# Kernel optimization log

Hardware: AMD Instinct MI355X
Metric: run time of the kernel (lower is better)

## Reference

```python
import jax, jax.numpy as jnp
import numpy as np

N_NODES = 50000
N_EDGES = 1000000
IN_DIM, HID_DIM, OUT_DIM = 128, 64, 16


def setup_inputs() -> dict:
    key = jax.random.key(0)
    k1, k2, k3, k4 = jax.random.split(key, 4)
    x = jax.random.normal(k1, (N_NODES, IN_DIM), dtype=jnp.float32)
    edge_index = jax.random.randint(k2, (2, N_EDGES), 0, N_NODES, dtype=jnp.int64)
    # Glorot-style scaling for weights, zero bias (PyG GCNConv default init style)
    W1 = jax.random.normal(k3, (IN_DIM, HID_DIM), dtype=jnp.float32) * (1.0 / np.sqrt(IN_DIM))
    b1 = jnp.zeros((HID_DIM,), dtype=jnp.float32)
    W2 = jax.random.normal(k4, (HID_DIM, OUT_DIM), dtype=jnp.float32) * (1.0 / np.sqrt(HID_DIM))
    b2 = jnp.zeros((OUT_DIM,), dtype=jnp.float32)
    return {"x": x, "edge_index": edge_index, "W1": W1, "b1": b1, "W2": W2, "b2": b2}


def gcn_conv(x, src, dst, W, b, num_nodes):
    """PyG GCNConv: add self loops, symmetric deg^{-1/2} normalization,
    linear transform, gather-scale-scatter aggregation, bias."""
    # degree includes self loops (src/dst already augmented by caller)
    deg = jax.ops.segment_sum(jnp.ones_like(dst, dtype=x.dtype), dst, num_segments=num_nodes)
    dinv = jnp.where(deg > 0, deg ** -0.5, 0.0)
    norm = dinv[src] * dinv[dst]            # [E']
    h = x @ W                                # [N, F_out] transform before aggregation
    msg = h[src] * norm[:, None]             # gather + scale
    out = jax.ops.segment_sum(msg, dst, num_segments=num_nodes)  # scatter-add
    return out + b


def reference(x, edge_index, W1, b1, W2, b2):
    n = x.shape[0]
    loops = jnp.arange(n, dtype=edge_index.dtype)
    src = jnp.concatenate([edge_index[0], loops])
    dst = jnp.concatenate([edge_index[1], loops])
    h = gcn_conv(x, src, dst, W1, b1, n)
    h = jax.nn.relu(h)
    out = gcn_conv(h, src, dst, W2, b2, n)
    return out
```

## Files before the change

kernel.cpp:

```cpp
#include <hip/hip_runtime.h>

#define IN_DIM 128
#define HID_DIM 64
#define OUT_DIM 16

#define SSHIFT 7
#define SMASK 127
#define CHUNK 4096
#define CBLK 256
#define KPT (CHUNK / CBLK)
#define CAP 4096

#define G1N 64
#define G1S 132

static __device__ __forceinline__ unsigned short f2bf(float f) {
    unsigned u = __float_as_uint(f);
    unsigned r = u + 0x7fffu + ((u >> 16) & 1u);
    return (unsigned short)(r >> 16);
}
static __device__ __forceinline__ unsigned packbf2(float a, float b) {
    return (unsigned)f2bf(a) | ((unsigned)f2bf(b) << 16);
}
static __device__ __forceinline__ float bflo(unsigned v) { return __uint_as_float(v << 16); }
static __device__ __forceinline__ float bfhi(unsigned v) { return __uint_as_float(v & 0xffff0000u); }

__global__ __launch_bounds__(CBLK) void passC2(const int* __restrict__ src,
                                               const int* __restrict__ dst,
                                               int* __restrict__ gcnt,
                                               int* __restrict__ eb,
                                               int E, int NS) {
    __shared__ int cnt[512];
    __shared__ int bofs[512];
    int t = threadIdx.x;
    for (int s = t; s < NS; s += CBLK) cnt[s] = 0;
    __syncthreads();
    int base = blockIdx.x * CHUNK;
    int dreg[KPT];
    #pragma unroll
    for (int k = 0; k < KPT; ++k) {
        int i = base + k * CBLK + t;
        int d = -1;
        if (i < E) { d = dst[i]; atomicAdd(&cnt[d >> SSHIFT], 1); }
        dreg[k] = d;
    }
    __syncthreads();
    for (int s = t; s < NS; s += CBLK) {
        int c = cnt[s];
        bofs[s] = c ? atomicAdd(&gcnt[s], c) : 0;
        cnt[s] = 0;
    }
    __syncthreads();
    #pragma unroll
    for (int k = 0; k < KPT; ++k) {
        int i = base + k * CBLK + t;
        if (i < E) {
            int d = dreg[k];
            int s = d >> SSHIFT;
            int off = atomicAdd(&cnt[s], 1);
            eb[(size_t)s * CAP + bofs[s] + off] = src[i] | ((d & SMASK) << 17);
        }
    }
}

__global__ __launch_bounds__(256) void passD(const int* __restrict__ eb,
                                             const int* __restrict__ tot,
                                             int* __restrict__ csr_src,
                                             int* __restrict__ row_ptr,
                                             float* __restrict__ dinv,
                                             int N, int E, int NS) {
    __shared__ int red[256];
    __shared__ int deg[128], incl[128], cur[128];
    int s = blockIdx.x, t = threadIdx.x;
    if (t < 128) deg[t] = 0;
    int part = 0;
    for (int k = t; k < s; k += 256) part += tot[k];
    red[t] = part;
    __syncthreads();
    for (int off = 128; off >= 1; off >>= 1) {
        if (t < off) red[t] += red[t + off];
        __syncthreads();
    }
    int b0 = red[0];
    int cnt = tot[s];
    const size_t sbase = (size_t)s * CAP;
    for (int k = t; k < cnt; k += 256) atomicAdd(&deg[eb[sbase + k] >> 17], 1);
    __syncthreads();
    if (t < 128) incl[t] = deg[t];
    __syncthreads();
    for (int off = 1; off < 128; off <<= 1) {
        int tmp = 0;
        if (t < 128 && t >= off) tmp = incl[t - off];
        __syncthreads();
        if (t < 128) incl[t] += tmp;
        __syncthreads();
    }
    if (t < 128) {
        int loff = incl[t] - deg[t];
        cur[t] = b0 + loff;
        int n = (s << SSHIFT) + t;
        if (n < N) {
            row_ptr[n] = b0 + loff;
            dinv[n] = rsqrtf((float)(deg[t] + 1));
        }
    }
    if (s == NS - 1 && t == 0) row_ptr[N] = E;
    __syncthreads();
    for (int k = t; k < cnt; k += 256) {
        int v = eb[sbase + k];
        int dl = v >> 17;
        int p = atomicAdd(&cur[dl], 1);
        csr_src[p] = v & 0x1FFFF;
    }
}

__global__ __launch_bounds__(256) void gemm1_kernel(const float* __restrict__ x,
                                                    const float* __restrict__ W1,
                                                    const float* __restrict__ dinv,
                                                    unsigned* __restrict__ h1u, int N) {
    __shared__ __align__(16) float sW[IN_DIM * HID_DIM];
    __shared__ __align__(16) float sx[G1N * G1S];
    int t = threadIdx.x;
    int node0 = blockIdx.x * G1N;

    const float4* W4  = (const float4*)W1;
    float4*       sW4 = (float4*)sW;
    #pragma unroll
    for (int i = 0; i < 8; ++i) sW4[i * 256 + t] = W4[i * 256 + t];

    const float4* x4 = (const float4*)x;
    for (int i = t; i < G1N * 32; i += 256) {
        int r = i >> 5, c = i & 31;
        int n = node0 + r; if (n >= N) n = 0;
        *(float4*)(sx + r * G1S + c * 4) = x4[(size_t)n * 32 + c];
    }
    __syncthreads();

    int og = t & 15, ng = t >> 4;
    float a00=0.f,a01=0.f,a02=0.f,a03=0.f, a10=0.f,a11=0.f,a12=0.f,a13=0.f,
          a20=0.f,a21=0.f,a22=0.f,a23=0.f, a30=0.f,a31=0.f,a32=0.f,a33=0.f;
    const float* xr = sx + (ng << 2) * G1S;
    #pragma unroll 4
    for (int k = 0; k < IN_DIM; ++k) {
        float x0 = xr[k];
        float x1 = xr[G1S + k];
        float x2 = xr[2 * G1S + k];
        float x3 = xr[3 * G1S + k];
        float4 wv = ((const float4*)(sW + k * HID_DIM))[og];
        a00 = fmaf(x0, wv.x, a00); a01 = fmaf(x0, wv.y, a01);
        a02 = fmaf(x0, wv.z, a02); a03 = fmaf(x0, wv.w, a03);
        a10 = fmaf(x1, wv.x, a10); a11 = fmaf(x1, wv.y, a11);
        a12 = fmaf(x1, wv.z, a12); a13 = fmaf(x1, wv.w, a13);
        a20 = fmaf(x2, wv.x, a20); a21 = fmaf(x2, wv.y, a21);
        a22 = fmaf(x2, wv.z, a22); a23 = fmaf(x2, wv.w, a23);
        a30 = fmaf(x3, wv.x, a30); a31 = fmaf(x3, wv.y, a31);
        a32 = fmaf(x3, wv.z, a32); a33 = fmaf(x3, wv.w, a33);
    }

    int nb = node0 + (ng << 2);
#define G1_STORE(i, c0, c1, c2, c3)                                         \
    {                                                                       \
        int n = nb + i;                                                     \
        if (n <= N) {                                                       \
            float dn = (n < N) ? dinv[n] : 0.f;         \
            uint2 pv;                                                       \
            pv.x = packbf2(c0 * dn, c1 * dn);                               \
            pv.y = packbf2(c2 * dn, c3 * dn);                               \
            ((uint2*)(h1u + (size_t)n * 32))[og] = pv;                      \
        }                                                                   \
    }
    G1_STORE(0, a00, a01, a02, a03)
    G1_STORE(1, a10, a11, a12, a13)
    G1_STORE(2, a20, a21, a22, a23)
    G1_STORE(3, a30, a31, a32, a33)
#undef G1_STORE
}

__global__ __launch_bounds__(256) void agg1_kernel(const unsigned* __restrict__ h1u,
                                                   const int* __restrict__ row_ptr,
                                                   const int* __restrict__ csr_src,
                                                   const float* __restrict__ dinv,
                                                   const float* __restrict__ b1,
                                                   const float* __restrict__ W2,
                                                   unsigned* __restrict__ h2u, int N) {
    __shared__ __align__(16) float sW[OUT_DIM * 68];
    int t = threadIdx.x;
    for (int i = t; i < HID_DIM * OUT_DIM; i += 256) {
        int k = i >> 4, j = i & 15;
        sW[j * 68 + k] = W2[i];
    }
    __syncthreads();

    int lane = t & 63;
    int h  = lane >> 5;
    int l  = lane & 31;
    int es = l >> 3;
    int dg = l & 7;
    int n = blockIdx.x * 8 + ((t >> 6) << 1) + h;
    if (n > N) return;
    if (n == N) {
        if (l < 4) { uint2 z; z.x = 0u; z.y = 0u; ((uint2*)h2u)[(size_t)N * 4 + l] = z; }
        return;
    }

    int e0 = row_ptr[n], e1 = row_ptr[n + 1];
    const uint4* rb = (const uint4*)h1u;
    int sb = h << 5;

    float a0 = 0.f, a1 = 0.f, a2 = 0.f, a3 = 0.f,
          a4 = 0.f, a5 = 0.f, a6 = 0.f, a7 = 0.f;

    for (int base = e0 - 1; base < e1; base += 32) {
        int idx = base + l;
        int sld = N;
        if (idx == e0 - 1) sld = n;
        else if (idx < e1) sld = csr_src[idx];
        int lim = e1 - base;
        if (lim > 32) lim = 32;
        int nr = (lim + 3) >> 2;
        nr = (nr + 1) & ~1;
        for (int r = 0; r < nr; r += 2) {
            int sA = __shfl(sld, sb + ((r + 0) << 2) + es);
            int sB = __shfl(sld, sb + ((r + 1) << 2) + es);
            uint4 vA = rb[(size_t)sA * 8 + dg];
            uint4 vB = rb[(size_t)sB * 8 + dg];
            a0 += bflo(vA.x) + bflo(vB.x);
            a1 += bfhi(vA.x) + bfhi(vB.x);
            a2 += bflo(vA.y) + bflo(vB.y);
            a3 += bfhi(vA.y) + bfhi(vB.y);
            a4 += bflo(vA.z) + bflo(vB.z);
            a5 += bfhi(vA.z) + bfhi(vB.z);
            a6 += bflo(vA.w) + bflo(vB.w);
            a7 += bfhi(vA.w) + bfhi(vB.w);
        }
    }
    #pragma unroll
    for (int m = 8; m <= 16; m <<= 1) {
        a0 += __shfl_xor(a0, m); a1 += __shfl_xor(a1, m);
        a2 += __shfl_xor(a2, m); a3 += __shfl_xor(a3, m);
        a4 += __shfl_xor(a4, m); a5 += __shfl_xor(a5, m);
        a6 += __shfl_xor(a6, m); a7 += __shfl_xor(a7, m);
    }

    float dn = dinv[n];
    float4 bA = ((const float4*)b1)[2 * dg];
    float4 bB = ((const float4*)b1)[2 * dg + 1];
    float r0 = fmaxf(fmaf(dn, a0, bA.x), 0.f);
    float r1 = fmaxf(fmaf(dn, a1, bA.y), 0.f);
    float r2 = fmaxf(fmaf(dn, a2, bA.z), 0.f);
    float r3 = fmaxf(fmaf(dn, a3, bA.w), 0.f);
    float r4 = fmaxf(fmaf(dn, a4, bB.x), 0.f);
    float r5 = fmaxf(fmaf(dn, a5, bB.y), 0.f);
    float r6 = fmaxf(fmaf(dn, a6, bB.z), 0.f);
    float r7 = fmaxf(fmaf(dn, a7, bB.w), 0.f);

    const float* wb = sW + ((es << 2) * 68) + (dg << 3);
    float4 wA, wB2;
    wA = *(const float4*)(wb);        wB2 = *(const float4*)(wb + 4);
    float p0 = r0*wA.x + r1*wA.y + r2*wA.z + r3*wA.w + r4*wB2.x + r5*wB2.y + r6*wB2.z + r7*wB2.w;
    wA = *(const float4*)(wb + 68);   wB2 = *(const float4*)(wb + 72);
    float p1 = r0*wA.x + r1*wA.y + r2*wA.z + r3*wA.w + r4*wB2.x + r5*wB2.y + r6*wB2.z + r7*wB2.w;
    wA = *(const float4*)(wb + 136);  wB2 = *(const float4*)(wb + 140);
    float p2 = r0*wA.x + r1*wA.y + r2*wA.z + r3*wA.w + r4*wB2.x + r5*wB2.y + r6*wB2.z + r7*wB2.w;
    wA = *(const float4*)(wb + 204);  wB2 = *(const float4*)(wb + 208);
    float p3 = r0*wA.x + r1*wA.y + r2*wA.z + r3*wA.w + r4*wB2.x + r5*wB2.y + r6*wB2.z + r7*wB2.w;

    #pragma unroll
    for (int m = 1; m <= 4; m <<= 1) {
        p0 += __shfl_xor(p0, m); p1 += __shfl_xor(p1, m);
        p2 += __shfl_xor(p2, m); p3 += __shfl_xor(p3, m);
    }
    if (dg == 0) {
        uint2 pv;
        pv.x = packbf2(p0 * dn, p1 * dn);
        pv.y = packbf2(p2 * dn, p3 * dn);
        ((uint2*)h2u)[(size_t)n * 4 + es] = pv;
    }
}

__global__ __launch_bounds__(256) void agg2_kernel(const unsigned* __restrict__ h2u,
                                                   const int* __restrict__ row_ptr,
                                                   const int* __restrict__ csr_src,
                                                   const float* __restrict__ dinv,
                                                   const float* __restrict__ b2,
                                                   float* __restrict__ out, int N) {
    int t = threadIdx.x;
    int lane = t & 63;
    int h  = lane >> 4;
    int l  = lane & 15;
    int es = l >> 2;
    int dg = l & 3;
    int n = blockIdx.x * 16 + ((t >> 6) << 2) + h;
    if (n >= N) return;

    int e0 = row_ptr[n], e1 = row_ptr[n + 1];
    const uint2* rb = (const uint2*)h2u;
    int sb = h << 4;

    float a0 = 0.f, a1 = 0.f, a2 = 0.f, a3 = 0.f;

    for (int base = e0 - 1; base < e1; base += 16) {
        int idx = base + l;
        int sld = N;
        if (idx == e0 - 1) sld = n;
        else if (idx < e1) sld = csr_src[idx];
        int lim = e1 - base;
        if (lim > 16) lim = 16;
        int nr = (lim + 3) >> 2;
        nr = (nr + 1) & ~1;
        for (int r = 0; r < nr; r += 2) {
            int sA = __shfl(sld, sb + ((r + 0) << 2) + es);
            int sB = __shfl(sld, sb + ((r + 1) << 2) + es);
            uint2 vA = rb[(size_t)sA * 4 + dg];
            uint2 vB = rb[(size_t)sB * 4 + dg];
            a0 += bflo(vA.x) + bflo(vB.x);
            a1 += bfhi(vA.x) + bfhi(vB.x);
            a2 += bflo(vA.y) + bflo(vB.y);
            a3 += bfhi(vA.y) + bfhi(vB.y);
        }
    }
    #pragma unroll
    for (int m = 4; m <= 8; m <<= 1) {
        a0 += __shfl_xor(a0, m); a1 += __shfl_xor(a1, m);
        a2 += __shfl_xor(a2, m); a3 += __shfl_xor(a3, m);
    }
    if (es == 0) {
        float dn = dinv[n];
        float4 bb = ((const float4*)b2)[dg];
        float4 r;
        r.x = fmaf(dn, a0, bb.x);
        r.y = fmaf(dn, a1, bb.y);
        r.z = fmaf(dn, a2, bb.z);
        r.w = fmaf(dn, a3, bb.w);
        ((float4*)out)[(size_t)n * 4 + dg] = r;
    }
}

extern "C" void kernel_launch(void* const* d_in, const int* in_sizes, int n_in,
                              void* d_out, int out_size, void* d_ws, size_t ws_size,
                              hipStream_t stream) {
    const float* x  = (const float*)d_in[0];
    const int*   ei = (const int*)d_in[1];
    const float* W1 = (const float*)d_in[2];
    const float* b1 = (const float*)d_in[3];
    const float* W2 = (const float*)d_in[4];
    const float* b2 = (const float*)d_in[5];
    float* out = (float*)d_out;

    const int N = in_sizes[0] / IN_DIM;
    const int E = in_sizes[1] / 2;
    const int* src = ei;
    const int* dst = ei + E;

    const int NS  = (N + SMASK) >> SSHIFT;
    const int NSP = NS + 1;
    const int BC  = (E + CHUNK - 1) / CHUNK;

    char* w = (char*)d_ws;
    auto alloc = [&](size_t bytes) -> void* {
        void* p = (void*)w;
        w += (bytes + 255) & ~(size_t)255;
        return p;
    };
    int*      gcnt    = (int*)     alloc((size_t)NSP * 4);
    int*      eb      = (int*)     alloc((size_t)NS * CAP * 4);
    int*      csr_src = (int*)     alloc((size_t)E * 4);
    int*      row_ptr = (int*)     alloc((size_t)(N + 1) * 4);
    float*    dinv    = (float*)   alloc((size_t)N * 4);
    unsigned* h1u     = (unsigned*)alloc((size_t)(N + 1) * 32 * 4);
    unsigned* h2u     = (unsigned*)alloc((size_t)(N + 1) * 8 * 4);

    const int GB  = (N + G1N) / G1N;
    const int AB1 = (N + 8) / 8;
    const int AB2 = (N + 15) / 16;

    hipMemsetAsync(gcnt, 0, (size_t)NSP * 4, stream);
    passC2<<<BC, CBLK, 0, stream>>>(src, dst, gcnt, eb, E, NS);
    passD <<<NS, 256,  0, stream>>>(eb, gcnt, csr_src, row_ptr, dinv, N, E, NS);

    gemm1_kernel<<<GB, 256, 0, stream>>>(x, W1, dinv, h1u, N);
    agg1_kernel<<<AB1, 256, 0, stream>>>(h1u, row_ptr, csr_src, dinv, b1, W2, h2u, N);
    agg2_kernel<<<AB2, 256, 0, stream>>>(h2u, row_ptr, csr_src, dinv, b2, out, N);
}
```

Before: 163.2 us.

## Fuse CSR finalisation with first GEMM via global degree atomics and block specialisation

Per-node degrees are now counted with global atomics inside the bucketing pass, so the first-layer GEMM no longer has to wait for the CSR build to produce dinv. The CSR-finalise kernel and the GEMM are merged into one launch, with blocks split by index between the two roles so they run concurrently. The GEMM tile shrinks to 32 nodes per block to spread more blocks. This removes a launch and a serialisation point, but adds a million global atomics to the bucketing pass and gives the fused kernel a large shared-memory footprint that may lower occupancy for the CSR blocks.

```diff
diff --git a/kernel.cpp b/kernel.cpp
--- a/kernel.cpp
+++ b/kernel.cpp
@@ -11,7 +11,7 @@
 #define KPT (CHUNK / CBLK)
 #define CAP 4096
 
-#define G1N 64
+#define G1N 32
 #define G1S 132
 
 static __device__ __forceinline__ unsigned short f2bf(float f) {
@@ -28,6 +28,7 @@
 __global__ __launch_bounds__(CBLK) void passC2(const int* __restrict__ src,
                                                const int* __restrict__ dst,
                                                int* __restrict__ gcnt,
+                                               int* __restrict__ deg,
                                                int* __restrict__ eb,
                                                int E, int NS) {
     __shared__ int cnt[512];
@@ -41,7 +42,11 @@
     for (int k = 0; k < KPT; ++k) {
         int i = base + k * CBLK + t;
         int d = -1;
-        if (i < E) { d = dst[i]; atomicAdd(&cnt[d >> SSHIFT], 1); }
+        if (i < E) {
+            d = dst[i];
+            atomicAdd(&cnt[d >> SSHIFT], 1);
+            atomicAdd(&deg[d], 1);
+        }
         dreg[k] = d;
     }
     __syncthreads();
@@ -63,117 +68,110 @@
     }
 }
 
-__global__ __launch_bounds__(256) void passD(const int* __restrict__ eb,
-                                             const int* __restrict__ tot,
-                                             int* __restrict__ csr_src,
-                                             int* __restrict__ row_ptr,
-                                             float* __restrict__ dinv,
-                                             int N, int E, int NS) {
+__global__ __launch_bounds__(256) void passDG(const int* __restrict__ eb,
+                                              const int* __restrict__ tot,
+                                              const int* __restrict__ deg,
+                                              const float* __restrict__ x,
+                                              const float* __restrict__ W1,
+                                              int* __restrict__ csr_src,
+                                              int* __restrict__ row_ptr,
+                                              float* __restrict__ dinv,
+                                              unsigned* __restrict__ h1u,
+                                              int N, int E, int NS) {
     __shared__ int red[256];
-    __shared__ int deg[128], incl[128], cur[128];
-    int s = blockIdx.x, t = threadIdx.x;
-    if (t < 128) deg[t] = 0;
-    int part = 0;
-    for (int k = t; k < s; k += 256) part += tot[k];
-    red[t] = part;
-    __syncthreads();
-    for (int off = 128; off >= 1; off >>= 1) {
-        if (t < off) red[t] += red[t + off];
-        __syncthreads();
-    }
-    int b0 = red[0];
-    int cnt = tot[s];
-    const size_t sbase = (size_t)s * CAP;
-    for (int k = t; k < cnt; k += 256) atomicAdd(&deg[eb[sbase + k] >> 17], 1);
-    __syncthreads();
-    if (t < 128) incl[t] = deg[t];
-    __syncthreads();
-    for (int off = 1; off < 128; off <<= 1) {
-        int tmp = 0;
-        if (t < 128 && t >= off) tmp = incl[t - off];
-        __syncthreads();
-        if (t < 128) incl[t] += tmp;
-        __syncthreads();
-    }
-    if (t < 128) {
-        int loff = incl[t] - deg[t];
-        cur[t] = b0 + loff;
-        int n = (s << SSHIFT) + t;
-        if (n < N) {
-            row_ptr[n] = b0 + loff;
-            dinv[n] = rsqrtf((float)(deg[t] + 1));
-        }
-    }
-    if (s == NS - 1 && t == 0) row_ptr[N] = E;
-    __syncthreads();
-    for (int k = t; k < cnt; k += 256) {
-        int v = eb[sbase + k];
-        int dl = v >> 17;
-        int p = atomicAdd(&cur[dl], 1);
-        csr_src[p] = v & 0x1FFFF;
-    }
-}
-
-__global__ __launch_bounds__(256) void gemm1_kernel(const float* __restrict__ x,
-                                                    const float* __restrict__ W1,
-                                                    const float* __restrict__ dinv,
-                                                    unsigned* __restrict__ h1u, int N) {
+    __shared__ int degS[128], incl[128], cur[128];
     __shared__ __align__(16) float sW[IN_DIM * HID_DIM];
     __shared__ __align__(16) float sx[G1N * G1S];
     int t = threadIdx.x;
-    int node0 = blockIdx.x * G1N;
-
-    const float4* W4  = (const float4*)W1;
-    float4*       sW4 = (float4*)sW;
-    #pragma unroll
-    for (int i = 0; i < 8; ++i) sW4[i * 256 + t] = W4[i * 256 + t];
-
-    const float4* x4 = (const float4*)x;
-    for (int i = t; i < G1N * 32; i += 256) {
-        int r = i >> 5, c = i & 31;
-        int n = node0 + r; if (n >= N) n = 0;
-        *(float4*)(sx + r * G1S + c * 4) = x4[(size_t)n * 32 + c];
-    }
-    __syncthreads();
-
-    int og = t & 15, ng = t >> 4;
-    float a00=0.f,a01=0.f,a02=0.f,a03=0.f, a10=0.f,a11=0.f,a12=0.f,a13=0.f,
-          a20=0.f,a21=0.f,a22=0.f,a23=0.f, a30=0.f,a31=0.f,a32=0.f,a33=0.f;
-    const float* xr = sx + (ng << 2) * G1S;
-    #pragma unroll 4
-    for (int k = 0; k < IN_DIM; ++k) {
-        float x0 = xr[k];
-        float x1 = xr[G1S + k];
-        float x2 = xr[2 * G1S + k];
-        float x3 = xr[3 * G1S + k];
-        float4 wv = ((const float4*)(sW + k * HID_DIM))[og];
-        a00 = fmaf(x0, wv.x, a00); a01 = fmaf(x0, wv.y, a01);
-        a02 = fmaf(x0, wv.z, a02); a03 = fmaf(x0, wv.w, a03);
-        a10 = fmaf(x1, wv.x, a10); a11 = fmaf(x1, wv.y, a11);
-        a12 = fmaf(x1, wv.z, a12); a13 = fmaf(x1, wv.w, a13);
-        a20 = fmaf(x2, wv.x, a20); a21 = fmaf(x2, wv.y, a21);
-        a22 = fmaf(x2, wv.z, a22); a23 = fmaf(x2, wv.w, a23);
-        a30 = fmaf(x3, wv.x, a30); a31 = fmaf(x3, wv.y, a31);
-        a32 = fmaf(x3, wv.z, a32); a33 = fmaf(x3, wv.w, a33);
-    }
-
-    int nb = node0 + (ng << 2);
+    int b = blockIdx.x;
+
+    if (b < NS) {
+        int s = b;
+        if (t < 128) degS[t] = 0;
+        int part = 0;
+        for (int k = t; k < s; k += 256) part += tot[k];
+        red[t] = part;
+        __syncthreads();
+        for (int off = 128; off >= 1; off >>= 1) {
+            if (t < off) red[t] += red[t + off];
+            __syncthreads();
+        }
+        int b0 = red[0];
+        int cnt = tot[s];
+        const size_t sbase = (size_t)s * CAP;
+        for (int k = t; k < cnt; k += 256) atomicAdd(&degS[eb[sbase + k] >> 17], 1);
+        __syncthreads();
+        if (t < 128) incl[t] = degS[t];
+        __syncthreads();
+        for (int off = 1; off < 128; off <<= 1) {
+            int tmp = 0;
+            if (t < 128 && t >= off) tmp = incl[t - off];
+            __syncthreads();
+            if (t < 128) incl[t] += tmp;
+            __syncthreads();
+        }
+        if (t < 128) {
+            int loff = incl[t] - degS[t];
+            cur[t] = b0 + loff;
+            int n = (s << SSHIFT) + t;
+            if (n < N) row_ptr[n] = b0 + loff;
+        }
+        if (s == NS - 1 && t == 0) row_ptr[N] = E;
+        __syncthreads();
+        for (int k = t; k < cnt; k += 256) {
+            int v = eb[sbase + k];
+            int dl = v >> 17;
+            int p = atomicAdd(&cur[dl], 1);
+            csr_src[p] = v & 0x1FFFF;
+        }
+    } else {
+        int node0 = (b - NS) * G1N;
+
+        const float4* W4  = (const float4*)W1;
+        float4*       sW4 = (float4*)sW;
+        #pragma unroll
+        for (int i = 0; i < 8; ++i) sW4[i * 256 + t] = W4[i * 256 + t];
+
+        const float4* x4 = (const float4*)x;
+        for (int i = t; i < G1N * 32; i += 256) {
+            int r = i >> 5, c = i & 31;
+            int n = node0 + r; if (n >= N) n = 0;
+            *(float4*)(sx + r * G1S + c * 4) = x4[(size_t)n * 32 + c];
+        }
+        __syncthreads();
+
+        int og = t & 15, ng = t >> 4;
+        float a00=0.f,a01=0.f,a02=0.f,a03=0.f,
+              a10=0.f,a11=0.f,a12=0.f,a13=0.f;
+        const float* xr = sx + (ng << 1) * G1S;
+        #pragma unroll 4
+        for (int k = 0; k < IN_DIM; ++k) {
+            float x0 = xr[k];
+            float x1 = xr[G1S + k];
+            float4 wv = ((const float4*)(sW + k * HID_DIM))[og];
+            a00 = fmaf(x0, wv.x, a00); a01 = fmaf(x0, wv.y, a01);
+            a02 = fmaf(x0, wv.z, a02); a03 = fmaf(x0, wv.w, a03);
+            a10 = fmaf(x1, wv.x, a10); a11 = fmaf(x1, wv.y, a11);
+            a12 = fmaf(x1, wv.z, a12); a13 = fmaf(x1, wv.w, a13);
+        }
+
+        int nb = node0 + (ng << 1);
 #define G1_STORE(i, c0, c1, c2, c3)                                         \
-    {                                                                       \
-        int n = nb + i;                                                     \
-        if (n <= N) {                                                       \
-            float dn = (n < N) ? dinv[n] : 0.f;         \
-            uint2 pv;                                                       \
-            pv.x = packbf2(c0 * dn, c1 * dn);                               \
-            pv.y = packbf2(c2 * dn, c3 * dn);                               \
-            ((uint2*)(h1u + (size_t)n * 32))[og] = pv;                      \
-        }                                                                   \
-    }
-    G1_STORE(0, a00, a01, a02, a03)
-    G1_STORE(1, a10, a11, a12, a13)
-    G1_STORE(2, a20, a21, a22, a23)
-    G1_STORE(3, a30, a31, a32, a33)
+        {                                                                   \
+            int n = nb + i;                                                 \
+            if (n <= N) {                                                   \
+                float dn = (n < N) ? rsqrtf((float)(deg[n] + 1)) : 0.f;     \
+                uint2 pv;                                                   \
+                pv.x = packbf2(c0 * dn, c1 * dn);                           \
+                pv.y = packbf2(c2 * dn, c3 * dn);                           \
+                ((uint2*)(h1u + (size_t)n * 32))[og] = pv;                  \
+                if (og == 0 && n < N) dinv[n] = dn;                         \
+            }                                                               \
+        }
+        G1_STORE(0, a00, a01, a02, a03)
+        G1_STORE(1, a10, a11, a12, a13)
 #undef G1_STORE
+    }
 }
 
 __global__ __launch_bounds__(256) void agg1_kernel(const unsigned* __restrict__ h1u,
@@ -363,6 +361,7 @@
         return p;
     };
     int*      gcnt    = (int*)     alloc((size_t)NSP * 4);
+    int*      deg     = (int*)     alloc((size_t)N * 4);
     int*      eb      = (int*)     alloc((size_t)NS * CAP * 4);
     int*      csr_src = (int*)     alloc((size_t)E * 4);
     int*      row_ptr = (int*)     alloc((size_t)(N + 1) * 4);
@@ -374,11 +373,11 @@
     const int AB1 = (N + 8) / 8;
     const int AB2 = (N + 15) / 16;
 
-    hipMemsetAsync(gcnt, 0, (size_t)NSP * 4, stream);
-    passC2<<<BC, CBLK, 0, stream>>>(src, dst, gcnt, eb, E, NS);
-    passD <<<NS, 256,  0, stream>>>(eb, gcnt, csr_src, row_ptr, dinv, N, E, NS);
-
-    gemm1_kernel<<<GB, 256, 0, stream>>>(x, W1, dinv, h1u, N);
+    size_t zbytes = (size_t)((char*)deg - (char*)gcnt) + (size_t)N * 4;
+    hipMemsetAsync(gcnt, 0, zbytes, stream);
+    passC2<<<BC, CBLK, 0, stream>>>(src, dst, gcnt, deg, eb, E, NS);
+    passDG<<<NS + GB, 256, 0, stream>>>(eb, gcnt, deg, x, W1,
+                                        csr_src, row_ptr, dinv, h1u, N, E, NS);
     agg1_kernel<<<AB1, 256, 0, stream>>>(h1u, row_ptr, csr_src, dinv, b1, W2, h2u, N);
     agg2_kernel<<<AB2, 256, 0, stream>>>(h2u, row_ptr, csr_src, dinv, b2, out, N);
 }
```

Result: slower. 193.0 us (+18.3%).
